# Kernel optimization log

Measured on AMD Instinct MI355X. Metric: run time of the kernel, lower is better.

Reference implementation:

```python
import jax, jax.numpy as jnp
import numpy as np

NUM_EXPERTS = 8
TOP_K = 2
D_MODEL = 1024
D_FF = 4096
B, S = 2, 2048


def setup_inputs() -> dict:
    key = jax.random.key(0)
    k1, k2, k3, k4 = jax.random.split(key, 4)
    scale_in = 1.0 / np.sqrt(D_MODEL)
    scale_ff = 1.0 / np.sqrt(D_FF)
    return {
        "hidden_states": jax.random.normal(k1, (B, S, D_MODEL), dtype=jnp.float32),
        "gate_w": jax.random.normal(k2, (D_MODEL, NUM_EXPERTS), dtype=jnp.float32) * scale_in,
        "w1": jax.random.normal(k3, (NUM_EXPERTS, D_MODEL, D_FF), dtype=jnp.float32) * scale_in,
        "w2": jax.random.normal(k4, (NUM_EXPERTS, D_FF, D_MODEL), dtype=jnp.float32) * scale_ff,
    }


def reference(hidden_states, gate_w, w1, w2):
    b, s, d = hidden_states.shape
    x = hidden_states.reshape(-1, d)                      # [T, d]
    gate_logits = x @ gate_w                              # [T, E]
    top_vals, top_idx = jax.lax.top_k(gate_logits, TOP_K)  # [T, K]
    # softmax over selected expert logits in fp32, cast back
    top_w = jax.nn.softmax(top_vals.astype(jnp.float32), axis=1).astype(x.dtype)
    # per-token per-expert combine weight: sum_k w[t,k] * (sel[t,k]==e)
    combine = jnp.einsum("tke,tk->te", jax.nn.one_hot(top_idx, NUM_EXPERTS, dtype=x.dtype), top_w)  # [T, E]
    # naive dense MoE: every expert over all tokens (matches torch loop)
    h = jax.nn.relu(jnp.einsum("td,edf->etf", x, w1))     # [E, T, d_ff]
    expert_out = jnp.einsum("etf,efd->etd", h, w2)        # [E, T, d]
    final = jnp.einsum("etd,te->td", expert_out, combine)  # [T, d]
    return final.reshape(b, s, d)
```

## Files before the change

kernel.cpp:

```cpp
#include <hip/hip_runtime.h>
#include <hip/hip_bf16.h>
#include <stdint.h>


#define T_TOK 4096
#define DM 1024
#define DF 4096
#define NE 8
#define BM 128
#define BN 128
#define BK 64
#define MAX_TILES 72
#define PAIR_CAP 9216

typedef __bf16 bf16x8 __attribute__((ext_vector_type(8)));
typedef float f32x4 __attribute__((ext_vector_type(4)));
typedef unsigned short ushort_t;

__device__ __forceinline__ ushort_t f2bf(float f) {
  uint32_t u = __float_as_uint(f);
  u += 0x7FFFu + ((u >> 16) & 1u);
  return (ushort_t)(u >> 16);
}

#define W1T_OFF 0ull
#define W2T_OFF 67108864ull
#define XB_OFF  134217728ull
#define H_OFF   142606336ull
#define RT_OFF  218103808ull
#define RO_COUNTS   0
#define RO_NTILES   96
#define RO_TILE_E   128
#define RO_TILE_S   448
#define RO_TILE_R   768
#define RO_PTOK     1088
#define RO_PW       37952
#define RO_TOPI     74816
#define RO_TOPW     107584
#define RT_BYTES    140352ull
#define WS_NEEDED   (RT_OFF + RT_BYTES)

__device__ __forceinline__ int xcd_work(int b, int live) {
  int k = b & 7, j = b >> 3;
  int q = live >> 3, r = live & 7;
  int cnt = q + (k < r ? 1 : 0);
  if (j >= cnt) return -1;
  int start = k * q + (k < r ? k : r);
  return start + j;
}

__global__ void gate_kernel(const float* __restrict__ x, const float* __restrict__ gw,
                            int* __restrict__ counts, int* __restrict__ topi,
                            float* __restrict__ topw, ushort_t* __restrict__ xb) {
  int wave = threadIdx.x >> 6;
  int lane = threadIdx.x & 63;
  int t = blockIdx.x * 4 + wave;
  const float* xr = x + (size_t)t * DM;
  ushort_t* xbr = xb + (size_t)t * DM;
  float acc[NE];
#pragma unroll
  for (int e = 0; e < NE; ++e) acc[e] = 0.f;
#pragma unroll
  for (int it = 0; it < DM / 256; ++it) {
    int d0 = (it * 64 + lane) * 4;
    float4 v = *(const float4*)&xr[d0];
    ushort4 o = { f2bf(v.x), f2bf(v.y), f2bf(v.z), f2bf(v.w) };
    *(ushort4*)&xbr[d0] = o;
    const float* g0 = gw + (size_t)d0 * NE;
#pragma unroll
    for (int e = 0; e < NE; ++e)
      acc[e] += v.x * g0[e] + v.y * g0[NE + e] + v.z * g0[2 * NE + e] + v.w * g0[3 * NE + e];
  }
#pragma unroll
  for (int off = 32; off > 0; off >>= 1) {
#pragma unroll
    for (int e = 0; e < NE; ++e) acc[e] += __shfl_xor(acc[e], off, 64);
  }
  if (lane == 0) {
    int i0 = 0; float v0 = acc[0];
#pragma unroll
    for (int e = 1; e < NE; ++e) if (acc[e] > v0) { v0 = acc[e]; i0 = e; }
    int i1 = -1; float v1 = -1e30f;
#pragma unroll
    for (int e = 0; e < NE; ++e) if (e != i0 && acc[e] > v1) { v1 = acc[e]; i1 = e; }
    float e1 = expf(v1 - v0);
    float w0 = 1.f / (1.f + e1);
    float w1 = e1 / (1.f + e1);
    topi[t * 2] = i0; topi[t * 2 + 1] = i1;
    topw[t * 2] = w0; topw[t * 2 + 1] = w1;
    atomicAdd(&counts[i0], 1);
    atomicAdd(&counts[i1], 1);
  }
}

__global__ void route_kernel(const int* __restrict__ counts,
                             const int* __restrict__ topi, const float* __restrict__ topw,
                             int* __restrict__ n_tiles, int* __restrict__ tile_e,
                             int* __restrict__ tile_s, int* __restrict__ tile_r,
                             int* __restrict__ ptok, float* __restrict__ pw) {
  __shared__ int loff[NE];
  __shared__ int lcur[NE];
  if (threadIdx.x == 0) {
    int off = 0, nt = 0;
    for (int e = 0; e < NE; ++e) {
      loff[e] = off;
      lcur[e] = 0;
      int c = counts[e];
      for (int m0 = 0; m0 < c; m0 += BM) {
        tile_e[nt] = e;
        tile_s[nt] = off + m0;
        tile_r[nt] = (c - m0 < BM) ? (c - m0) : BM;
        ++nt;
      }
      off += ((c + BM - 1) / BM) * BM;
    }
    *n_tiles = nt;
  }
  __syncthreads();
  for (int t = threadIdx.x; t < T_TOK; t += 256) {
#pragma unroll
    for (int k = 0; k < 2; ++k) {
      int e = topi[t * 2 + k];
      int pos = atomicAdd(&lcur[e], 1);
      int p = loff[e] + pos;
      ptok[p] = t;
      pw[p] = topw[t * 2 + k];
    }
  }
}

__global__ void transpose_all(const float* __restrict__ w1, const float* __restrict__ w2,
                              ushort_t* __restrict__ w1t, ushort_t* __restrict__ w2t) {
  __shared__ ushort_t tile[64][136];
  int b = blockIdx.x;
  const float* src; ushort_t* dst; int R, C, bx, by, e;
  if (b < 4096) {
    e = b >> 9; int t2 = b & 511;
    bx = t2 & 63; by = t2 >> 6;
    src = w1; dst = w1t; R = DM; C = DF;
  } else {
    b -= 4096;
    e = b >> 9; int t2 = b & 511;
    bx = t2 & 15; by = t2 >> 4;
    src = w2; dst = w2t; R = DF; C = DM;
  }
  src += (size_t)e * R * C;
  dst += (size_t)e * R * C;
  int c0 = bx * 64, r0 = by * 128;
  int tr = threadIdx.x >> 4;
  int tc = (threadIdx.x & 15) << 2;
#pragma unroll
  for (int i = 0; i < 8; ++i) {
    int r = i * 16 + tr;
    float4 v = *(const float4*)&src[(size_t)(r0 + r) * C + c0 + tc];
    tile[tc + 0][r] = f2bf(v.x);
    tile[tc + 1][r] = f2bf(v.y);
    tile[tc + 2][r] = f2bf(v.z);
    tile[tc + 3][r] = f2bf(v.w);
  }
  __syncthreads();
  int cr = threadIdx.x >> 5;
  int rg = (threadIdx.x & 31) << 2;
#pragma unroll
  for (int j = 0; j < 8; ++j) {
    int c = j * 8 + cr;
    ushort4 o = { tile[c][rg], tile[c][rg + 1], tile[c][rg + 2], tile[c][rg + 3] };
    *(ushort4*)&dst[(size_t)(c0 + c) * R + r0 + rg] = o;
  }
}


#define GLD(srcp, dstp)                                                        \
  __builtin_amdgcn_global_load_lds(                                            \
      (const __attribute__((address_space(1))) void*)(srcp),                   \
      (__attribute__((address_space(3))) void*)(dstp), 16, 0, 0)

__device__ __forceinline__ void gemm_core(
    ushort_t* As, ushort_t* Bs,
    const ushort_t* const (&a_sp)[4], const ushort_t* const (&b_sp)[4],
    int NT, int wid, int lane, f32x4 (&acc)[4][4]) {
  int fr = lane & 15, ch = lane >> 4, sw = lane & 7;
  int k0s = (ch ^ sw) * 8;
  int k1s = ((ch + 4) ^ sw) * 8;
  int m_off = (wid >> 1) * 64, n_off = (wid & 1) * 64;
  int abase = (m_off + fr) * 64;
  int bbase = (n_off + fr) * 64;

  for (int t = 0; t < NT; ++t) {
    int k0 = t * BK;
#pragma unroll
    for (int j = 0; j < 4; ++j) {
      GLD(a_sp[j] + k0, As + (wid * 4 + j) * 512);
      GLD(b_sp[j] + k0, Bs + (wid * 4 + j) * 512);
    }
    asm volatile("s_waitcnt vmcnt(0)" ::: "memory");
    __syncthreads();

#pragma unroll
    for (int kx = 0; kx < 2; ++kx) {
      int ks = kx ? k1s : k0s;
      bf16x8 af[4], bf[4];
#pragma unroll
      for (int mi = 0; mi < 4; ++mi) af[mi] = *(const bf16x8*)&As[abase + mi * 1024 + ks];
#pragma unroll
      for (int ni = 0; ni < 4; ++ni) bf[ni] = *(const bf16x8*)&Bs[bbase + ni * 1024 + ks];
#pragma unroll
      for (int mi = 0; mi < 4; ++mi)
#pragma unroll
        for (int ni = 0; ni < 4; ++ni)
          acc[mi][ni] = __builtin_amdgcn_mfma_f32_16x16x32_bf16(af[mi], bf[ni], acc[mi][ni], 0, 0, 0);
    }
    __syncthreads();
  }
}

__global__ __launch_bounds__(256, 4) void gemm1_kernel(
    const ushort_t* __restrict__ xb, const ushort_t* __restrict__ w1t,
    ushort_t* __restrict__ h,
    const int* __restrict__ n_tiles, const int* __restrict__ tile_e,
    const int* __restrict__ tile_s, const int* __restrict__ tile_r,
    const int* __restrict__ ptok) {
  int nt = *n_tiles;
  int ntp = (nt + 3) & ~3;
  int w = xcd_work(blockIdx.x, ntp * 32);
  if (w < 0) return;
  int g = w >> 5, r = w & 31;
  int tg = g >> 2, ng = g & 3;
  int tile = tg * 4 + (r & 3);
  if (tile >= nt) return;
  int n0 = (ng * 8 + (r >> 2)) * BN;
  int e = tile_e[tile], p0 = tile_s[tile], rows = tile_r[tile];

  __shared__ ushort_t As[BM * BK];
  __shared__ ushort_t Bs[BN * BK];
  int tid = threadIdx.x, wid = tid >> 6, lane = tid & 63;
  int lr = lane >> 3;
  int swc = (lane & 7) ^ (lr & 7);

  const ushort_t* a_sp[4];
  const ushort_t* b_sp[4];
#pragma unroll
  for (int j = 0; j < 4; ++j) {
    int rr = wid * 32 + j * 8 + lr;
    int tok = (rr < rows) ? ptok[p0 + rr] : 0;
    a_sp[j] = xb + (size_t)tok * DM + swc * 8;
    b_sp[j] = w1t + ((size_t)e * DF + n0 + rr) * DM + swc * 8;
  }

  f32x4 acc[4][4] = {};
  gemm_core(As, Bs, a_sp, b_sp, DM / BK, wid, lane, acc);

  int m_off = (wid >> 1) * 64, n_off = (wid & 1) * 64;
  int col = lane & 15, rq = (lane >> 4) * 4;
#pragma unroll
  for (int mi = 0; mi < 4; ++mi)
#pragma unroll
    for (int rr = 0; rr < 4; ++rr) {
      int m = m_off + mi * 16 + rq + rr;
      bool valid = m < rows;
      size_t rowoff = (size_t)(p0 + m) * DF + n0 + n_off;
#pragma unroll
      for (int ni = 0; ni < 4; ++ni) {
        float v = acc[mi][ni][rr];
        v = valid ? (v > 0.f ? v : 0.f) : 0.f;
        h[rowoff + ni * 16 + col] = f2bf(v);
      }
    }
}

__global__ __launch_bounds__(256, 4) void gemm2_kernel(
    const ushort_t* __restrict__ h, const ushort_t* __restrict__ w2t,
    float* __restrict__ out,
    const int* __restrict__ n_tiles, const int* __restrict__ tile_e,
    const int* __restrict__ tile_s, const int* __restrict__ tile_r,
    const int* __restrict__ ptok, const float* __restrict__ pw) {
  int nt = *n_tiles;
  int ntp = (nt + 1) & ~1;
  int w = xcd_work(blockIdx.x, ntp * 8);
  if (w < 0) return;
  int g = w >> 2, r = w & 3;
  int tg = g >> 2, ng = g & 3;
  int tile = tg * 2 + (r & 1);
  if (tile >= nt) return;
  int n0 = (ng * 2 + (r >> 1)) * BN;
  int e = tile_e[tile], p0 = tile_s[tile], rows = tile_r[tile];

  __shared__ ushort_t As[BM * BK];
  __shared__ ushort_t Bs[BN * BK];
  int tid = threadIdx.x, wid = tid >> 6, lane = tid & 63;
  int lr = lane >> 3;
  int swc = (lane & 7) ^ (lr & 7);

  const ushort_t* a_sp[4];
  const ushort_t* b_sp[4];
#pragma unroll
  for (int j = 0; j < 4; ++j) {
    int rr = wid * 32 + j * 8 + lr;
    a_sp[j] = h + (size_t)(p0 + rr) * DF + swc * 8;
    b_sp[j] = w2t + ((size_t)e * DM + n0 + rr) * DF + swc * 8;
  }

  f32x4 acc[4][4] = {};
  gemm_core(As, Bs, a_sp, b_sp, DF / BK, wid, lane, acc);

  int m_off = (wid >> 1) * 64, n_off = (wid & 1) * 64;
  int col = lane & 15, rq = (lane >> 4) * 4;
#pragma unroll
  for (int mi = 0; mi < 4; ++mi)
#pragma unroll
    for (int rr = 0; rr < 4; ++rr) {
      int m = m_off + mi * 16 + rq + rr;
      if (m < rows) {
        int p = p0 + m;
        int tok = ptok[p];
        float wgt = pw[p];
        size_t o = (size_t)tok * DM + n0 + n_off;
#pragma unroll
        for (int ni = 0; ni < 4; ++ni)
          atomicAdd(&out[o + ni * 16 + col], wgt * acc[mi][ni][rr]);
      }
    }
}

extern "C" void kernel_launch(void* const* d_in, const int* in_sizes, int n_in,
                              void* d_out, int out_size, void* d_ws, size_t ws_size,
                              hipStream_t stream) {
  const float* x  = (const float*)d_in[0];
  const float* gw = (const float*)d_in[1];
  const float* w1 = (const float*)d_in[2];
  const float* w2 = (const float*)d_in[3];
  float* out = (float*)d_out;
  char* ws = (char*)d_ws;
  if (ws_size < WS_NEEDED) return;

  ushort_t* w1t = (ushort_t*)(ws + W1T_OFF);
  ushort_t* w2t = (ushort_t*)(ws + W2T_OFF);
  ushort_t* xb  = (ushort_t*)(ws + XB_OFF);
  ushort_t* h   = (ushort_t*)(ws + H_OFF);
  char* rt = ws + RT_OFF;
  int*   counts  = (int*)(rt + RO_COUNTS);
  int*   n_tiles = (int*)(rt + RO_NTILES);
  int*   tile_e  = (int*)(rt + RO_TILE_E);
  int*   tile_s  = (int*)(rt + RO_TILE_S);
  int*   tile_r  = (int*)(rt + RO_TILE_R);
  int*   ptok    = (int*)(rt + RO_PTOK);
  float* pw      = (float*)(rt + RO_PW);
  int*   topi    = (int*)(rt + RO_TOPI);
  float* topw    = (float*)(rt + RO_TOPW);

  hipMemsetAsync(rt, 0, 128, stream);
  hipMemsetAsync(out, 0, (size_t)T_TOK * DM * sizeof(float), stream);

  hipLaunchKernelGGL(gate_kernel, dim3(T_TOK / 4), dim3(256), 0, stream,
                     x, gw, counts, topi, topw, xb);
  hipLaunchKernelGGL(route_kernel, dim3(1), dim3(256), 0, stream,
                     counts, topi, topw, n_tiles, tile_e, tile_s, tile_r, ptok, pw);
  hipLaunchKernelGGL(transpose_all, dim3(8192), dim3(256), 0, stream,
                     w1, w2, w1t, w2t);
  hipLaunchKernelGGL(gemm1_kernel, dim3(MAX_TILES * 32), dim3(256), 0, stream,
                     xb, w1t, h, n_tiles, tile_e, tile_s, tile_r, ptok);
  hipLaunchKernelGGL(gemm2_kernel, dim3(MAX_TILES * 8), dim3(256), 0, stream,
                     h, w2t, out, n_tiles, tile_e, tile_s, tile_r, ptok, pw);
}
```

Before: 384.1 us.

## Fuse weight transposes into gate and gemm1 kernels to overlap work

```diff
diff --git a/kernel.cpp b/kernel.cpp
--- a/kernel.cpp
+++ b/kernel.cpp
@@ -12,6 +12,7 @@
 #define BK 64
 #define MAX_TILES 72
 #define PAIR_CAP 9216
+#define G1_GRID (MAX_TILES * 32)
 
 typedef __bf16 bf16x8 __attribute__((ext_vector_type(8)));
 typedef float f32x4 __attribute__((ext_vector_type(4)));
@@ -49,12 +50,51 @@
   return start + j;
 }
 
-__global__ void gate_kernel(const float* __restrict__ x, const float* __restrict__ gw,
-                            int* __restrict__ counts, int* __restrict__ topi,
-                            float* __restrict__ topw, ushort_t* __restrict__ xb) {
+__device__ __forceinline__ void transpose_tile(
+    ushort_t* sh, const float* __restrict__ src, ushort_t* __restrict__ dst,
+    int R, int C, int bx, int by, int e) {
+  src += (size_t)e * R * C;
+  dst += (size_t)e * R * C;
+  int c0 = bx * 64, r0 = by * 128;
+  int tr = threadIdx.x >> 4;
+  int tc = (threadIdx.x & 15) << 2;
+#pragma unroll
+  for (int i = 0; i < 8; ++i) {
+    int r = i * 16 + tr;
+    float4 v = *(const float4*)&src[(size_t)(r0 + r) * C + c0 + tc];
+    sh[(tc + 0) * 136 + r] = f2bf(v.x);
+    sh[(tc + 1) * 136 + r] = f2bf(v.y);
+    sh[(tc + 2) * 136 + r] = f2bf(v.z);
+    sh[(tc + 3) * 136 + r] = f2bf(v.w);
+  }
+  __syncthreads();
+  int cr = threadIdx.x >> 5;
+  int rg = (threadIdx.x & 31) << 2;
+#pragma unroll
+  for (int j = 0; j < 8; ++j) {
+    int c = j * 8 + cr;
+    ushort4 o = { sh[c * 136 + rg], sh[c * 136 + rg + 1],
+                  sh[c * 136 + rg + 2], sh[c * 136 + rg + 3] };
+    *(ushort4*)&dst[(size_t)(c0 + c) * R + r0 + rg] = o;
+  }
+}
+
+__global__ __launch_bounds__(256) void gate_w1t_kernel(
+    const float* __restrict__ x, const float* __restrict__ gw,
+    int* __restrict__ counts, int* __restrict__ topi,
+    float* __restrict__ topw, ushort_t* __restrict__ xb,
+    const float* __restrict__ w1, ushort_t* __restrict__ w1t) {
+  __shared__ ushort_t sh[8704];
+  int b = blockIdx.x;
+  if (b >= 1024) {
+    int t = b - 1024;
+    int e = t >> 9, t2 = t & 511;
+    transpose_tile(sh, w1, w1t, DM, DF, t2 & 63, t2 >> 6, e);
+    return;
+  }
   int wave = threadIdx.x >> 6;
   int lane = threadIdx.x & 63;
-  int t = blockIdx.x * 4 + wave;
+  int t = b * 4 + wave;
   const float* xr = x + (size_t)t * DM;
   ushort_t* xbr = xb + (size_t)t * DM;
   float acc[NE];
@@ -85,9 +125,9 @@
     for (int e = 0; e < NE; ++e) if (e != i0 && acc[e] > v1) { v1 = acc[e]; i1 = e; }
     float e1 = expf(v1 - v0);
     float w0 = 1.f / (1.f + e1);
-    float w1 = e1 / (1.f + e1);
+    float w1s = e1 / (1.f + e1);
     topi[t * 2] = i0; topi[t * 2 + 1] = i1;
-    topw[t * 2] = w0; topw[t * 2 + 1] = w1;
+    topw[t * 2] = w0; topw[t * 2 + 1] = w1s;
     atomicAdd(&counts[i0], 1);
     atomicAdd(&counts[i1], 1);
   }
@@ -129,46 +169,6 @@
   }
 }
 
-__global__ void transpose_all(const float* __restrict__ w1, const float* __restrict__ w2,
-                              ushort_t* __restrict__ w1t, ushort_t* __restrict__ w2t) {
-  __shared__ ushort_t tile[64][136];
-  int b = blockIdx.x;
-  const float* src; ushort_t* dst; int R, C, bx, by, e;
-  if (b < 4096) {
-    e = b >> 9; int t2 = b & 511;
-    bx = t2 & 63; by = t2 >> 6;
-    src = w1; dst = w1t; R = DM; C = DF;
-  } else {
-    b -= 4096;
-    e = b >> 9; int t2 = b & 511;
-    bx = t2 & 15; by = t2 >> 4;
-    src = w2; dst = w2t; R = DF; C = DM;
-  }
-  src += (size_t)e * R * C;
-  dst += (size_t)e * R * C;
-  int c0 = bx * 64, r0 = by * 128;
-  int tr = threadIdx.x >> 4;
-  int tc = (threadIdx.x & 15) << 2;
-#pragma unroll
-  for (int i = 0; i < 8; ++i) {
-    int r = i * 16 + tr;
-    float4 v = *(const float4*)&src[(size_t)(r0 + r) * C + c0 + tc];
-    tile[tc + 0][r] = f2bf(v.x);
-    tile[tc + 1][r] = f2bf(v.y);
-    tile[tc + 2][r] = f2bf(v.z);
-    tile[tc + 3][r] = f2bf(v.w);
-  }
-  __syncthreads();
-  int cr = threadIdx.x >> 5;
-  int rg = (threadIdx.x & 31) << 2;
-#pragma unroll
-  for (int j = 0; j < 8; ++j) {
-    int c = j * 8 + cr;
-    ushort4 o = { tile[c][rg], tile[c][rg + 1], tile[c][rg + 2], tile[c][rg + 3] };
-    *(ushort4*)&dst[(size_t)(c0 + c) * R + r0 + rg] = o;
-  }
-}
-
 
 #define GLD(srcp, dstp)                                                        \
   __builtin_amdgcn_global_load_lds(                                            \
@@ -214,15 +214,24 @@
   }
 }
 
-__global__ __launch_bounds__(256, 4) void gemm1_kernel(
+__global__ __launch_bounds__(256, 4) void gemm1_w2t_kernel(
     const ushort_t* __restrict__ xb, const ushort_t* __restrict__ w1t,
     ushort_t* __restrict__ h,
     const int* __restrict__ n_tiles, const int* __restrict__ tile_e,
     const int* __restrict__ tile_s, const int* __restrict__ tile_r,
-    const int* __restrict__ ptok) {
+    const int* __restrict__ ptok,
+    const float* __restrict__ w2, ushort_t* __restrict__ w2t) {
+  __shared__ ushort_t sh[BM * BK + BN * BK];
+  int b = blockIdx.x;
+  if (b >= G1_GRID) {
+    int t = b - G1_GRID;
+    int e = t >> 9, t2 = t & 511;
+    transpose_tile(sh, w2, w2t, DF, DM, t2 & 15, t2 >> 4, e);
+    return;
+  }
   int nt = *n_tiles;
   int ntp = (nt + 3) & ~3;
-  int w = xcd_work(blockIdx.x, ntp * 32);
+  int w = xcd_work(b, ntp * 32);
   if (w < 0) return;
   int g = w >> 5, r = w & 31;
   int tg = g >> 2, ng = g & 3;
@@ -231,8 +240,8 @@
   int n0 = (ng * 8 + (r >> 2)) * BN;
   int e = tile_e[tile], p0 = tile_s[tile], rows = tile_r[tile];
 
-  __shared__ ushort_t As[BM * BK];
-  __shared__ ushort_t Bs[BN * BK];
+  ushort_t* As = sh;
+  ushort_t* Bs = sh + BM * BK;
   int tid = threadIdx.x, wid = tid >> 6, lane = tid & 63;
   int lr = lane >> 3;
   int swc = (lane & 7) ^ (lr & 7);
@@ -351,14 +360,12 @@
   hipMemsetAsync(rt, 0, 128, stream);
   hipMemsetAsync(out, 0, (size_t)T_TOK * DM * sizeof(float), stream);
 
-  hipLaunchKernelGGL(gate_kernel, dim3(T_TOK / 4), dim3(256), 0, stream,
-                     x, gw, counts, topi, topw, xb);
+  hipLaunchKernelGGL(gate_w1t_kernel, dim3(1024 + 4096), dim3(256), 0, stream,
+                     x, gw, counts, topi, topw, xb, w1, w1t);
   hipLaunchKernelGGL(route_kernel, dim3(1), dim3(256), 0, stream,
                      counts, topi, topw, n_tiles, tile_e, tile_s, tile_r, ptok, pw);
-  hipLaunchKernelGGL(transpose_all, dim3(8192), dim3(256), 0, stream,
-                     w1, w2, w1t, w2t);
-  hipLaunchKernelGGL(gemm1_kernel, dim3(MAX_TILES * 32), dim3(256), 0, stream,
-                     xb, w1t, h, n_tiles, tile_e, tile_s, tile_r, ptok);
+  hipLaunchKernelGGL(gemm1_w2t_kernel, dim3(G1_GRID + 4096), dim3(256), 0, stream,
+                     xb, w1t, h, n_tiles, tile_e, tile_s, tile_r, ptok, w2, w2t);
   hipLaunchKernelGGL(gemm2_kernel, dim3(MAX_TILES * 8), dim3(256), 0, stream,
                      h, w2t, out, n_tiles, tile_e, tile_s, tile_r, ptok, pw);
 }
```

After: 367.6 us. 4.3% less time.
